# Optimization experiments

Hardware: AMD Instinct MI355X
Metric: run time of the kernel (lower is better)

The kernel has to match this reference:

```python
import jax, jax.numpy as jnp
import numpy as np

S, B, C = 56, 5, 20
N = 128


def _cxcywh_to_xyxy(b):
    cx, cy, w, h = b[..., 0], b[..., 1], b[..., 2], b[..., 3]
    return jnp.stack([cx - 0.5 * w, cy - 0.5 * h, cx + 0.5 * w, cy + 0.5 * h], axis=-1)


def setup_inputs() -> dict:
    key = jax.random.key(0)
    k1, k2, k3 = jax.random.split(key, 3)
    predicts_tensor = jax.random.normal(k1, (N, S, S, B, C + 5), dtype=jnp.float32)
    targets_tensor = jax.random.uniform(k2, (N, S, S, C + 5), dtype=jnp.float32)
    anchors = jax.random.uniform(k3, (B, 2), dtype=jnp.float32)
    return {"predicts_tensor": predicts_tensor, "targets_tensor": targets_tensor, "anchors": anchors}


def reference(predicts_tensor, targets_tensor, anchors):
    p = predicts_tensor.reshape(-1, S, S, B, C + 5)
    # decode: sigmoid on cx,cy ; exp * anchor on w,h
    xy = jax.nn.sigmoid(p[..., C + 1:C + 3])
    wh = jnp.exp(p[..., C + 3:]) * anchors  # anchors [B,2] broadcasts over [...,B,2]
    p = jnp.concatenate([p[..., :C + 1], xy, wh], axis=-1)

    pb = _cxcywh_to_xyxy(p[..., C + 1:])                         # [N,S,S,B,4]
    tb = _cxcywh_to_xyxy(targets_tensor[..., C + 1:])[..., None, :]  # [N,S,S,1,4]

    # torchvision box_iou, vectorized over all cells and B boxes
    lt = jnp.maximum(pb[..., :2], tb[..., :2])
    rb = jnp.minimum(pb[..., 2:], tb[..., 2:])
    whi = jnp.clip(rb - lt, 0.0)
    inter = whi[..., 0] * whi[..., 1]
    area_p = (pb[..., 2] - pb[..., 0]) * (pb[..., 3] - pb[..., 1])
    area_t = (tb[..., 2] - tb[..., 0]) * (tb[..., 3] - tb[..., 1])
    ious = inter / (area_p + area_t - inter)                     # [N,S,S,B]

    best_idx = jnp.argmax(ious, axis=-1)                         # [N,S,S]
    pbest = jnp.take_along_axis(p, best_idx[..., None, None], axis=3)[..., 0, :]  # [N,S,S,C+5]
    pbest = pbest.at[..., 0].set(pbest[..., 0] * best_idx.astype(pbest.dtype))

    exists = targets_tensor[..., C:C + 1]
    sse = lambda a, b: jnp.sum((a - b) ** 2)  # MSELoss(reduction='sum')

    loss_xcyc = sse(exists * pbest[..., C + 1:C + 3], exists * targets_tensor[..., C + 1:C + 3])
    p_wh = pbest[..., C + 3:]
    p_wh = jnp.sign(p_wh) * jnp.sqrt(jnp.abs(p_wh) + 1e-6)
    loss_wh = sse(exists * p_wh, exists * targets_tensor[..., C + 3:])
    loss_cls = sse(exists * pbest[..., :C], exists * targets_tensor[..., :C])
    loss_obj = sse(exists * pbest[..., C:C + 1], exists * targets_tensor[..., C:C + 1])
    noobj = 1.0 - exists
    loss_noobj = sse(noobj * pbest[..., C:C + 1], noobj * targets_tensor[..., C:C + 1])

    return loss_xcyc + loss_wh + loss_cls + loss_noobj + loss_obj
```

## Files before the change

kernel.cpp:

```cpp
#include <hip/hip_runtime.h>

constexpr int S_   = 56;
constexpr int B_   = 5;
constexpr int C_   = 20;
constexpr int N_   = 128;
constexpr int CELLS = N_ * S_ * S_;
constexpr int PSTR  = B_ * (C_ + 5);
constexpr int TSTR  = C_ + 5;

constexpr int GC    = 64;
constexpr int GPB   = 4;
constexpr int NBLK  = CELLS / (GC * GPB);
constexpr int GP_B  = GC * PSTR * 4;
constexpr int GT_B  = GC * TSTR * 4;
constexpr int GRP_B = GP_B + GT_B;

__device__ __forceinline__ void gload_lds16(const char* g, char* l) {
    __builtin_amdgcn_global_load_lds(
        (const __attribute__((address_space(1))) void*)g,
        (__attribute__((address_space(3))) void*)l,
        16, 0, 0);
}

#define WAITVM(N) asm volatile("s_waitcnt vmcnt(" #N ")" ::: "memory")

__device__ __forceinline__ void stage_group(const float* __restrict__ pred,
                                            const float* __restrict__ targ,
                                            int g, char* buf, int lane) {
    const char* gp = (const char*)(pred + (size_t)g * GC * PSTR);
    const char* gt = (const char*)(targ + (size_t)g * GC * TSTR);
    #pragma unroll
    for (int it = 0; it < 31; ++it)
        gload_lds16(gp + it * 1024 + lane * 16, buf + it * 1024);
    if (lane < 16)
        gload_lds16(gp + 31744 + lane * 16, buf + 31744);
    #pragma unroll
    for (int it = 0; it < 6; ++it)
        gload_lds16(gt + it * 1024 + lane * 16, buf + GP_B + it * 1024);
    if (lane < 16)
        gload_lds16(gt + 6144 + lane * 16, buf + GP_B + 6144);
}

__device__ __forceinline__ float cell_loss(const char* buf, int lane,
                                           const float* aw, const float* ah) {
    const float* pc = (const float*)buf + (size_t)lane * PSTR;
    const float* tp = (const float*)(buf + GP_B) + (size_t)lane * TSTR;

    const float tcx = tp[C_ + 1], tcy = tp[C_ + 2];
    const float tw  = tp[C_ + 3], th  = tp[C_ + 4];
    const float tx0 = tcx - 0.5f * tw, ty0 = tcy - 0.5f * th;
    const float tx1 = tcx + 0.5f * tw, ty1 = tcy + 0.5f * th;
    const float area_t = tw * th;

    float best_iou = -1.f;
    int   best_b = 0;
    float bcx = 0.f, bcy = 0.f, bw = 0.f, bh = 0.f;

    #pragma unroll
    for (int b = 0; b < B_; ++b) {
        const float rcx = pc[b * TSTR + C_ + 1];
        const float rcy = pc[b * TSTR + C_ + 2];
        const float rw  = pc[b * TSTR + C_ + 3];
        const float rh  = pc[b * TSTR + C_ + 4];

        const float cx = __builtin_amdgcn_rcpf(1.f + __expf(-rcx));
        const float cy = __builtin_amdgcn_rcpf(1.f + __expf(-rcy));
        const float w  = __expf(rw) * aw[b];
        const float h  = __expf(rh) * ah[b];

        const float x0 = cx - 0.5f * w, y0 = cy - 0.5f * h;
        const float x1 = cx + 0.5f * w, y1 = cy + 0.5f * h;

        float wi = fminf(x1, tx1) - fmaxf(x0, tx0);
        float hi = fminf(y1, ty1) - fmaxf(y0, ty0);
        wi = fmaxf(wi, 0.f);
        hi = fmaxf(hi, 0.f);
        const float inter = wi * hi;
        const float iou = inter * __builtin_amdgcn_rcpf(w * h + area_t - inter);

        const bool better = iou > best_iou;
        best_iou = better ? iou : best_iou;
        best_b   = better ? b   : best_b;
        bcx = better ? cx : bcx;
        bcy = better ? cy : bcy;
        bw  = better ? w  : bw;
        bh  = better ? h  : bh;
    }

    const float* pb = pc + best_b * TSTR;

    float acc = 0.f;
    #pragma unroll
    for (int k = 0; k < C_; ++k) {
        float v = pb[k];
        if (k == 0) v *= (float)best_b;
        const float d = v - tp[k];
        acc = fmaf(d, d, acc);
    }

    float d;
    d = bcx - tcx; acc = fmaf(d, d, acc);
    d = bcy - tcy; acc = fmaf(d, d, acc);

    d = sqrtf(bw + 1e-6f) - tw; acc = fmaf(d, d, acc);
    d = sqrtf(bh + 1e-6f) - th; acc = fmaf(d, d, acc);

    const float e    = tp[C_];
    const float ne   = 1.f - e;
    const float dobj = pb[C_] - e;
    return e * e * acc + (e * e + ne * ne) * (dobj * dobj);
}

__global__ __launch_bounds__(64) void yolo_loss_kernel(
    const float* __restrict__ pred,
    const float* __restrict__ targ,
    const float* __restrict__ anch,
    float* __restrict__ part)
{
    __shared__ char lds[2 * GRP_B];

    const int lane = threadIdx.x;
    const int g0   = blockIdx.x * GPB;

    float aw[B_], ah[B_];
    #pragma unroll
    for (int b = 0; b < B_; ++b) { aw[b] = anch[2 * b]; ah[b] = anch[2 * b + 1]; }

    stage_group(pred, targ, g0 + 0, lds,         lane);
    stage_group(pred, targ, g0 + 1, lds + GRP_B, lane);

    float total = 0.f;

    WAITVM(39);
    total += cell_loss(lds,         lane, aw, ah);
    stage_group(pred, targ, g0 + 2, lds,         lane);

    WAITVM(39);
    total += cell_loss(lds + GRP_B, lane, aw, ah);
    stage_group(pred, targ, g0 + 3, lds + GRP_B, lane);

    WAITVM(39);
    total += cell_loss(lds,         lane, aw, ah);

    WAITVM(0);
    total += cell_loss(lds + GRP_B, lane, aw, ah);

    #pragma unroll
    for (int off = 32; off > 0; off >>= 1)
        total += __shfl_down(total, off, 64);

    if (lane == 0)
        part[blockIdx.x] = total;
}

__global__ __launch_bounds__(1024) void finalize_kernel(
    const float* __restrict__ part, float* __restrict__ out)
{
    float v = 0.f;
    for (int i = threadIdx.x; i < NBLK; i += 1024)
        v += part[i];

    #pragma unroll
    for (int off = 32; off > 0; off >>= 1)
        v += __shfl_down(v, off, 64);

    __shared__ float ws[16];
    if ((threadIdx.x & 63) == 0) ws[threadIdx.x >> 6] = v;
    __syncthreads();
    if (threadIdx.x < 16) {
        float x = ws[threadIdx.x];
        #pragma unroll
        for (int off = 8; off > 0; off >>= 1)
            x += __shfl_down(x, off, 16);
        if (threadIdx.x == 0) out[0] = x;
    }
}

extern "C" void kernel_launch(void* const* d_in, const int* in_sizes, int n_in,
                              void* d_out, int out_size, void* d_ws, size_t ws_size,
                              hipStream_t stream) {
    const float* pred = (const float*)d_in[0];
    const float* targ = (const float*)d_in[1];
    const float* anch = (const float*)d_in[2];
    float* out  = (float*)d_out;
    float* part = (float*)d_ws;

    yolo_loss_kernel<<<NBLK, 64, 0, stream>>>(pred, targ, anch, part);
    finalize_kernel<<<1, 1024, 0, stream>>>(part, out);
}
```

Measured before the change: 304.8 us.

## Use 16-cell groups with a 14-stage double-buffered loop over fewer blocks

Measured after the change: 307.1 us. Within noise of the previous version (+0.8%).

```diff
diff --git a/kernel.cpp b/kernel.cpp
--- a/kernel.cpp
+++ b/kernel.cpp
@@ -8,12 +8,13 @@
 constexpr int PSTR  = B_ * (C_ + 5);
 constexpr int TSTR  = C_ + 5;
 
-constexpr int GC    = 64;
-constexpr int GPB   = 4;
-constexpr int NBLK  = CELLS / (GC * GPB);
-constexpr int GP_B  = GC * PSTR * 4;
-constexpr int GT_B  = GC * TSTR * 4;
-constexpr int GRP_B = GP_B + GT_B;
+constexpr int GCELL  = 16;
+constexpr int NGROUP = CELLS / GCELL;
+constexpr int GRID   = 1792;
+constexpr int GPBK   = NGROUP / GRID;
+constexpr int GP_B   = GCELL * PSTR * 4;
+constexpr int GT_B   = GCELL * TSTR * 4;
+constexpr int BUF_B  = GP_B + GT_B;
 
 __device__ __forceinline__ void gload_lds16(const char* g, char* l) {
     __builtin_amdgcn_global_load_lds(
@@ -27,18 +28,16 @@
 __device__ __forceinline__ void stage_group(const float* __restrict__ pred,
                                             const float* __restrict__ targ,
                                             int g, char* buf, int lane) {
-    const char* gp = (const char*)(pred + (size_t)g * GC * PSTR);
-    const char* gt = (const char*)(targ + (size_t)g * GC * TSTR);
+    const char* gp = (const char*)(pred + (size_t)g * GCELL * PSTR);
+    const char* gt = (const char*)(targ + (size_t)g * GCELL * TSTR);
     #pragma unroll
-    for (int it = 0; it < 31; ++it)
+    for (int it = 0; it < 7; ++it)
         gload_lds16(gp + it * 1024 + lane * 16, buf + it * 1024);
-    if (lane < 16)
-        gload_lds16(gp + 31744 + lane * 16, buf + 31744);
-    #pragma unroll
-    for (int it = 0; it < 6; ++it)
-        gload_lds16(gt + it * 1024 + lane * 16, buf + GP_B + it * 1024);
-    if (lane < 16)
-        gload_lds16(gt + 6144 + lane * 16, buf + GP_B + 6144);
+    if (lane < 52)
+        gload_lds16(gp + 7168 + lane * 16, buf + 7168);
+    gload_lds16(gt + lane * 16, buf + GP_B);
+    if (lane < 36)
+        gload_lds16(gt + 1024 + lane * 16, buf + GP_B + 1024);
 }
 
 __device__ __forceinline__ float cell_loss(const char* buf, int lane,
@@ -117,37 +116,40 @@
     const float* __restrict__ anch,
     float* __restrict__ part)
 {
-    __shared__ char lds[2 * GRP_B];
+    __shared__ char lds[2 * BUF_B];
 
     const int lane = threadIdx.x;
-    const int g0   = blockIdx.x * GPB;
+    const int g0   = blockIdx.x * GPBK;
+
+    char* bufA = lds;
+    char* bufB = lds + BUF_B;
 
     float aw[B_], ah[B_];
     #pragma unroll
     for (int b = 0; b < B_; ++b) { aw[b] = anch[2 * b]; ah[b] = anch[2 * b + 1]; }
 
-    stage_group(pred, targ, g0 + 0, lds,         lane);
-    stage_group(pred, targ, g0 + 1, lds + GRP_B, lane);
+    stage_group(pred, targ, g0 + 0, bufA, lane);
+    stage_group(pred, targ, g0 + 1, bufB, lane);
 
     float total = 0.f;
 
-    WAITVM(39);
-    total += cell_loss(lds,         lane, aw, ah);
-    stage_group(pred, targ, g0 + 2, lds,         lane);
-
-    WAITVM(39);
-    total += cell_loss(lds + GRP_B, lane, aw, ah);
-    stage_group(pred, targ, g0 + 3, lds + GRP_B, lane);
-
-    WAITVM(39);
-    total += cell_loss(lds,         lane, aw, ah);
-
+    #pragma unroll 1
+    for (int k = 0; k < 6; ++k) {
+        WAITVM(10);
+        if (lane < GCELL) total += cell_loss(bufA, lane, aw, ah);
+        stage_group(pred, targ, g0 + 2 * k + 2, bufA, lane);
+        WAITVM(10);
+        if (lane < GCELL) total += cell_loss(bufB, lane, aw, ah);
+        stage_group(pred, targ, g0 + 2 * k + 3, bufB, lane);
+    }
+    WAITVM(10);
+    if (lane < GCELL) total += cell_loss(bufA, lane, aw, ah);
     WAITVM(0);
-    total += cell_loss(lds + GRP_B, lane, aw, ah);
+    if (lane < GCELL) total += cell_loss(bufB, lane, aw, ah);
 
     #pragma unroll
-    for (int off = 32; off > 0; off >>= 1)
-        total += __shfl_down(total, off, 64);
+    for (int off = 8; off > 0; off >>= 1)
+        total += __shfl_down(total, off, 16);
 
     if (lane == 0)
         part[blockIdx.x] = total;
@@ -157,7 +159,7 @@
     const float* __restrict__ part, float* __restrict__ out)
 {
     float v = 0.f;
-    for (int i = threadIdx.x; i < NBLK; i += 1024)
+    for (int i = threadIdx.x; i < GRID; i += 1024)
         v += part[i];
 
     #pragma unroll
@@ -185,6 +187,6 @@
     float* out  = (float*)d_out;
     float* part = (float*)d_ws;
 
-    yolo_loss_kernel<<<NBLK, 64, 0, stream>>>(pred, targ, anch, part);
+    yolo_loss_kernel<<<GRID, 64, 0, stream>>>(pred, targ, anch, part);
     finalize_kernel<<<1, 1024, 0, stream>>>(part, out);
 }
```
